# Optimization experiments

Measured on AMD Instinct MI355X. Metric: run time of the kernel, lower is better.

The kernel has to match this reference:

```python
import jax, jax.numpy as jnp
import numpy as np


def setup_inputs() -> dict:
    key = jax.random.key(0)
    k1, k2, k3, k4 = jax.random.split(key, 4)
    N, S, F, UNITS = 50000, 32, 128, 128
    x = jax.random.normal(k1, (N, F), dtype=jnp.float32)
    neigh_x = jax.random.normal(k2, (N, S, F), dtype=jnp.float32)
    kernel_self = jax.random.normal(k3, (F, UNITS), dtype=jnp.float32) * 0.05
    kernel_neigh = jax.random.normal(k4, (F, UNITS), dtype=jnp.float32) * 0.05
    bias = jnp.zeros((2 * UNITS,), dtype=jnp.float32)
    return {"x": x, "neigh_x": neigh_x, "kernel_self": kernel_self,
            "kernel_neigh": kernel_neigh, "bias": bias}


def reference(x, neigh_x, kernel_self, kernel_neigh, bias):
    # neigh_x: [N, S, F]. Original transposes to [N, F, S] and applies
    # tf.raw_ops.NthElement with n = S//2 + S%2 (n-th smallest, 0-indexed)
    # along the last (neighbor) axis. Equivalent: sort along neighbor axis
    # of the untransposed tensor and take index n.
    S = neigh_x.shape[1]
    n = S // 2 + S % 2
    med = jnp.sort(neigh_x, axis=1)[:, n, :]  # [N, F]
    out = jnp.concatenate([x @ kernel_self, med @ kernel_neigh], axis=1)  # [N, 2*units] (concat=True)
    out = out + bias
    return jax.nn.relu(out)
```

## Files before the change

kernel.cpp:

```cpp
#include <hip/hip_runtime.h>

namespace {

typedef float f32x2 __attribute__((ext_vector_type(2)));
typedef float f32x4 __attribute__((ext_vector_type(4)));

constexpr int S   = 32;
constexpr int F   = 128;
constexpr int BR  = 32;
constexpr int TPB = 256;

struct CEPair { int a, b; };

constexpr int batcher_count16() {
  int n = 16, cnt = 0;
  for (int p = 1; p < n; p <<= 1)
    for (int k = p; k >= 1; k >>= 1)
      for (int j = k % p; j + k < n; j += 2 * k)
        for (int i = 0; i < k && i + j + k < n; ++i)
          if ((i + j) / (2 * p) == (i + j + k) / (2 * p))
            ++cnt;
  return cnt;
}
constexpr int NCE = batcher_count16();

struct Net16 { CEPair ce[NCE]; };

constexpr Net16 make_net16() {
  Net16 net{};
  int n = 16, c = 0;
  for (int p = 1; p < n; p <<= 1)
    for (int k = p; k >= 1; k >>= 1)
      for (int j = k % p; j + k < n; j += 2 * k)
        for (int i = 0; i < k && i + j + k < n; ++i)
          if ((i + j) / (2 * p) == (i + j + k) / (2 * p))
            net.ce[c++] = CEPair{i + j, i + j + k};
  return net;
}
constexpr Net16 NET16 = make_net16();

__device__ __forceinline__ f32x2 min2(f32x2 a, f32x2 b) {
  f32x2 r; r.x = fminf(a.x, b.x); r.y = fminf(a.y, b.y); return r;
}
__device__ __forceinline__ f32x2 max2(f32x2 a, f32x2 b) {
  f32x2 r; r.x = fmaxf(a.x, b.x); r.y = fmaxf(a.y, b.y); return r;
}

template<int T>
__device__ __forceinline__ void sort16(f32x2 (&v)[16]) {
  if constexpr (T < NCE) {
    constexpr int a = NET16.ce[T].a;
    constexpr int b = NET16.ce[T].b;
    f32x2 x = v[a], y = v[b];
    v[a] = min2(x, y);
    v[b] = max2(x, y);
    sort16<T + 1>(v);
  }
}

__global__ __launch_bounds__(TPB, 4) void fused_median_gemm(
    const float* __restrict__ x,
    const float* __restrict__ neigh,
    const float* __restrict__ Ks,
    const float* __restrict__ Kn,
    const float* __restrict__ bias,
    float* __restrict__ out,
    int N)
{
    __shared__ __align__(16) float xs[BR][F];
    __shared__ __align__(16) float ms[BR][F];

    const int tid  = threadIdx.x;
    const int row0 = blockIdx.x * BR;

    {
        const int lane = tid & 63;
        const int rp   = tid >> 6;
#pragma unroll 1
        for (int i = 0; i < BR; i += 4) {
            const int rl = i + rp;
            int row = row0 + rl;
            if (row > N - 1) row = N - 1;
            const f32x2* base =
                (const f32x2*)(neigh + (size_t)row * (S * F)) + lane;

            f32x2 A[16], B[16];
#pragma unroll
            for (int s = 0; s < 16; ++s)
                A[s] = __builtin_nontemporal_load(base + (size_t)s * 64);
#pragma unroll
            for (int s = 0; s < 16; ++s)
                B[s] = __builtin_nontemporal_load(base + (size_t)(16 + s) * 64);

            sort16<0>(A);
            sort16<0>(B);

            f32x2 c[16];
#pragma unroll
            for (int q = 0; q < 16; ++q) c[q] = max2(A[q], B[15 - q]);
#pragma unroll
            for (int st = 8; st >= 1; st >>= 1)
#pragma unroll
                for (int q = 0; q < st; ++q) c[q] = min2(c[q], c[q + st]);

            ((f32x2*)&ms[rl][0])[lane] = c[0];
            ((f32x2*)&xs[rl][0])[lane] =
                *((const f32x2*)(x + (size_t)row * F) + lane);
        }
    }
    __syncthreads();

    const int tu   = tid & 31;
    const int tr   = tid >> 5;
    const int ucol = tu * 8;
    const bool self_half = (tu < 16);
    const float* __restrict__ W = self_half ? Ks : Kn;
    const int ul = self_half ? ucol : (ucol - 128);
    const float* lin = self_half ? &xs[0][0] : &ms[0][0];

    f32x4 acc[4][2];
#pragma unroll
    for (int r = 0; r < 4; ++r) {
        acc[r][0] = f32x4{0.f, 0.f, 0.f, 0.f};
        acc[r][1] = f32x4{0.f, 0.f, 0.f, 0.f};
    }

    for (int f0 = 0; f0 < F; f0 += 4) {
        f32x4 wv[4][2];
#pragma unroll
        for (int df = 0; df < 4; ++df) {
            wv[df][0] = *(const f32x4*)&W[(f0 + df) * 128 + ul];
            wv[df][1] = *(const f32x4*)&W[(f0 + df) * 128 + ul + 4];
        }
        f32x4 xv[4];
#pragma unroll
        for (int r = 0; r < 4; ++r)
            xv[r] = *(const f32x4*)&lin[(tr * 4 + r) * F + f0];

#pragma unroll
        for (int r = 0; r < 4; ++r) {
#pragma unroll
            for (int df = 0; df < 4; ++df) {
                const float xc = xv[r][df];
#pragma unroll
                for (int h = 0; h < 2; ++h) {
                    acc[r][h].x = fmaf(xc, wv[df][h].x, acc[r][h].x);
                    acc[r][h].y = fmaf(xc, wv[df][h].y, acc[r][h].y);
                    acc[r][h].z = fmaf(xc, wv[df][h].z, acc[r][h].z);
                    acc[r][h].w = fmaf(xc, wv[df][h].w, acc[r][h].w);
                }
            }
        }
    }

    const f32x4 bv0 = *(const f32x4*)&bias[ucol];
    const f32x4 bv1 = *(const f32x4*)&bias[ucol + 4];
#pragma unroll
    for (int r = 0; r < 4; ++r) {
        const int row = row0 + tr * 4 + r;
        if (row < N) {
            f32x4 o0, o1;
            o0.x = fmaxf(acc[r][0].x + bv0.x, 0.f);
            o0.y = fmaxf(acc[r][0].y + bv0.y, 0.f);
            o0.z = fmaxf(acc[r][0].z + bv0.z, 0.f);
            o0.w = fmaxf(acc[r][0].w + bv0.w, 0.f);
            o1.x = fmaxf(acc[r][1].x + bv1.x, 0.f);
            o1.y = fmaxf(acc[r][1].y + bv1.y, 0.f);
            o1.z = fmaxf(acc[r][1].z + bv1.z, 0.f);
            o1.w = fmaxf(acc[r][1].w + bv1.w, 0.f);
            __builtin_nontemporal_store(o0, (f32x4*)&out[(size_t)row * 256 + ucol]);
            __builtin_nontemporal_store(o1, (f32x4*)&out[(size_t)row * 256 + ucol + 4]);
        }
    }
}

}

extern "C" void kernel_launch(void* const* d_in, const int* in_sizes, int n_in,
                              void* d_out, int out_size, void* d_ws, size_t ws_size,
                              hipStream_t stream) {
    const float* x     = (const float*)d_in[0];
    const float* neigh = (const float*)d_in[1];
    const float* Ks    = (const float*)d_in[2];
    const float* Kn    = (const float*)d_in[3];
    const float* bias  = (const float*)d_in[4];
    float* out = (float*)d_out;

    const int N = in_sizes[0] / F;
    const int grid = (N + BR - 1) / BR;
    hipLaunchKernelGGL(fused_median_gemm, dim3(grid), dim3(TPB), 0, stream,
                       x, neigh, Ks, Kn, bias, out, N);
}
```

Baseline: 197.0 us.

## Make each wavefront own eight rows and drop block-wide barrier

```diff
diff --git a/kernel.cpp b/kernel.cpp
--- a/kernel.cpp
+++ b/kernel.cpp
@@ -67,110 +67,94 @@
     float* __restrict__ out,
     int N)
 {
-    __shared__ __align__(16) float xs[BR][F];
-    __shared__ __align__(16) float ms[BR][F];
+    __shared__ __align__(16) float xs[4][8][F];
+    __shared__ __align__(16) float ms[4][8][F];
 
     const int tid  = threadIdx.x;
-    const int row0 = blockIdx.x * BR;
+    const int wv   = tid >> 6;
+    const int lane = tid & 63;
+    const int row0 = blockIdx.x * BR + wv * 8;
 
-    {
-        const int lane = tid & 63;
-        const int rp   = tid >> 6;
 #pragma unroll 1
-        for (int i = 0; i < BR; i += 4) {
-            const int rl = i + rp;
-            int row = row0 + rl;
-            if (row > N - 1) row = N - 1;
-            const f32x2* base =
-                (const f32x2*)(neigh + (size_t)row * (S * F)) + lane;
+    for (int r = 0; r < 8; ++r) {
+        int row = row0 + r;
+        if (row > N - 1) row = N - 1;
+        const f32x2* base =
+            (const f32x2*)(neigh + (size_t)row * (S * F)) + lane;
 
-            f32x2 A[16], B[16];
+        const f32x2 xv =
+            *((const f32x2*)(x + (size_t)row * F) + lane);
+
+        f32x2 A[16], B[16];
 #pragma unroll
-            for (int s = 0; s < 16; ++s)
-                A[s] = __builtin_nontemporal_load(base + (size_t)s * 64);
+        for (int s = 0; s < 16; ++s)
+            A[s] = __builtin_nontemporal_load(base + (size_t)s * 64);
 #pragma unroll
-            for (int s = 0; s < 16; ++s)
-                B[s] = __builtin_nontemporal_load(base + (size_t)(16 + s) * 64);
+        for (int s = 0; s < 16; ++s)
+            B[s] = __builtin_nontemporal_load(base + (size_t)(16 + s) * 64);
 
-            sort16<0>(A);
-            sort16<0>(B);
+        sort16<0>(A);
+        sort16<0>(B);
 
-            f32x2 c[16];
+        f32x2 c[16];
 #pragma unroll
-            for (int q = 0; q < 16; ++q) c[q] = max2(A[q], B[15 - q]);
+        for (int q = 0; q < 16; ++q) c[q] = max2(A[q], B[15 - q]);
 #pragma unroll
-            for (int st = 8; st >= 1; st >>= 1)
+        for (int st = 8; st >= 1; st >>= 1)
 #pragma unroll
-                for (int q = 0; q < st; ++q) c[q] = min2(c[q], c[q + st]);
+            for (int q = 0; q < st; ++q) c[q] = min2(c[q], c[q + st]);
 
-            ((f32x2*)&ms[rl][0])[lane] = c[0];
-            ((f32x2*)&xs[rl][0])[lane] =
-                *((const f32x2*)(x + (size_t)row * F) + lane);
-        }
-    }
-    __syncthreads();
-
-    const int tu   = tid & 31;
-    const int tr   = tid >> 5;
-    const int ucol = tu * 8;
-    const bool self_half = (tu < 16);
-    const float* __restrict__ W = self_half ? Ks : Kn;
-    const int ul = self_half ? ucol : (ucol - 128);
-    const float* lin = self_half ? &xs[0][0] : &ms[0][0];
-
-    f32x4 acc[4][2];
-#pragma unroll
-    for (int r = 0; r < 4; ++r) {
-        acc[r][0] = f32x4{0.f, 0.f, 0.f, 0.f};
-        acc[r][1] = f32x4{0.f, 0.f, 0.f, 0.f};
+        ((f32x2*)&ms[wv][r][0])[lane] = c[0];
+        ((f32x2*)&xs[wv][r][0])[lane] = xv;
     }
 
-    for (int f0 = 0; f0 < F; f0 += 4) {
-        f32x4 wv[4][2];
+    __threadfence_block();
+
+    const bool self_half = (lane < 32);
+    const float* __restrict__ W = self_half ? Ks : Kn;
+    const int wcol = (lane * 4) & 127;
+    const float* lin = self_half ? &xs[wv][0][0] : &ms[wv][0][0];
+
+    f32x4 acc[8];
 #pragma unroll
-        for (int df = 0; df < 4; ++df) {
-            wv[df][0] = *(const f32x4*)&W[(f0 + df) * 128 + ul];
-            wv[df][1] = *(const f32x4*)&W[(f0 + df) * 128 + ul + 4];
-        }
-        f32x4 xv[4];
+    for (int r = 0; r < 8; ++r) acc[r] = f32x4{0.f, 0.f, 0.f, 0.f};
+
+#pragma unroll 4
+    for (int k4 = 0; k4 < 32; ++k4) {
+        f32x4 wv4[4];
 #pragma unroll
-        for (int r = 0; r < 4; ++r)
-            xv[r] = *(const f32x4*)&lin[(tr * 4 + r) * F + f0];
+        for (int dk = 0; dk < 4; ++dk)
+            wv4[dk] = *(const f32x4*)&W[(k4 * 4 + dk) * 128 + wcol];
+
+        f32x4 xr[8];
+#pragma unroll
+        for (int r = 0; r < 8; ++r)
+            xr[r] = *(const f32x4*)&lin[r * F + k4 * 4];
 
 #pragma unroll
-        for (int r = 0; r < 4; ++r) {
+        for (int r = 0; r < 8; ++r) {
 #pragma unroll
-            for (int df = 0; df < 4; ++df) {
-                const float xc = xv[r][df];
-#pragma unroll
-                for (int h = 0; h < 2; ++h) {
-                    acc[r][h].x = fmaf(xc, wv[df][h].x, acc[r][h].x);
-                    acc[r][h].y = fmaf(xc, wv[df][h].y, acc[r][h].y);
-                    acc[r][h].z = fmaf(xc, wv[df][h].z, acc[r][h].z);
-                    acc[r][h].w = fmaf(xc, wv[df][h].w, acc[r][h].w);
-                }
+            for (int dk = 0; dk < 4; ++dk) {
+                const float s = xr[r][dk];
+                acc[r].x = fmaf(s, wv4[dk].x, acc[r].x);
+                acc[r].y = fmaf(s, wv4[dk].y, acc[r].y);
+                acc[r].z = fmaf(s, wv4[dk].z, acc[r].z);
+                acc[r].w = fmaf(s, wv4[dk].w, acc[r].w);
             }
         }
     }
 
-    const f32x4 bv0 = *(const f32x4*)&bias[ucol];
-    const f32x4 bv1 = *(const f32x4*)&bias[ucol + 4];
+    const f32x4 bv = *(const f32x4*)&bias[lane * 4];
 #pragma unroll
-    for (int r = 0; r < 4; ++r) {
-        const int row = row0 + tr * 4 + r;
-        if (row < N) {
-            f32x4 o0, o1;
-            o0.x = fmaxf(acc[r][0].x + bv0.x, 0.f);
-            o0.y = fmaxf(acc[r][0].y + bv0.y, 0.f);
-            o0.z = fmaxf(acc[r][0].z + bv0.z, 0.f);
-            o0.w = fmaxf(acc[r][0].w + bv0.w, 0.f);
-            o1.x = fmaxf(acc[r][1].x + bv1.x, 0.f);
-            o1.y = fmaxf(acc[r][1].y + bv1.y, 0.f);
-            o1.z = fmaxf(acc[r][1].z + bv1.z, 0.f);
-            o1.w = fmaxf(acc[r][1].w + bv1.w, 0.f);
-            __builtin_nontemporal_store(o0, (f32x4*)&out[(size_t)row * 256 + ucol]);
-            __builtin_nontemporal_store(o1, (f32x4*)&out[(size_t)row * 256 + ucol + 4]);
-        }
+    for (int r = 0; r < 8; ++r) {
+        int row = row0 + r;
+        if (row > N - 1) row = N - 1;
+        f32x4 o;
+        o.x = fmaxf(acc[r].x + bv.x, 0.f);
+        o.y = fmaxf(acc[r].y + bv.y, 0.f);
+        o.z = fmaxf(acc[r].z + bv.z, 0.f);
+        o.w = fmaxf(acc[r].w + bv.w, 0.f);
+        __builtin_nontemporal_store(o, (f32x4*)&out[(size_t)row * 256 + lane * 4]);
     }
 }
 
```

New measurement: 198.7 us. No clear change (+0.8%).
